# Kernel optimization log

Measured on AMD Instinct MI355X. Metric: run time of the kernel, lower is better.

## Reference

```python
import jax, jax.numpy as jnp
import numpy as np

H = 128  # hidden_dim


def gcn_conv(x, src, dst, n, W, b):
    """PyG GCNConv: add self-loops, symmetric norm, gather-transform-scatter."""
    h = x @ W  # [n, H]
    loop = jnp.arange(n, dtype=src.dtype)
    s = jnp.concatenate([src, loop])
    d = jnp.concatenate([dst, loop])
    deg = jax.ops.segment_sum(jnp.ones(s.shape[0], h.dtype), d, num_segments=n)
    dinv = jnp.where(deg > 0, jax.lax.rsqrt(deg), 0.0)
    norm = dinv[s] * dinv[d]  # [E+n]
    msg = h[s] * norm[:, None]
    out = jax.ops.segment_sum(msg, d, num_segments=n)
    return out + b


def encode(x, edge_index, batch, num_graphs, params):
    src, dst = edge_index[0], edge_index[1]
    n = x.shape[0]
    for (W, b) in params:
        x = jax.nn.relu(gcn_conv(x, src, dst, n, W, b))
    sums = jax.ops.segment_sum(x, batch, num_segments=num_graphs)
    cnts = jax.ops.segment_sum(jnp.ones((n, 1), x.dtype), batch, num_segments=num_graphs)
    return sums / jnp.maximum(cnts, 1.0)  # global_mean_pool -> [B, H]


def setup_inputs() -> dict:
    key = jax.random.key(0)
    ks = jax.random.split(key, 32)
    B, C = 32, 5
    Nd, Ed = 1280, 5120
    Np, Ep = 12800, 204800
    f32 = jnp.float32

    def lin(k, fan_in, fan_out):
        k1, k2 = jax.random.split(k)
        lim = 1.0 / np.sqrt(fan_in)
        W = jax.random.uniform(k1, (fan_in, fan_out), f32, -lim, lim)
        b = jax.random.uniform(k2, (fan_out,), f32, -lim, lim)
        return W, b

    Wd0, bd0 = lin(ks[0], 78, H)
    Wd1, bd1 = lin(ks[1], H, H)
    Wd2, bd2 = lin(ks[2], H, H)
    Wp0, bp0 = lin(ks[3], 1280, H)
    Wp1, bp1 = lin(ks[4], H, H)
    Wp2, bp2 = lin(ks[5], H, H)
    Wq, bq = lin(ks[6], H, H)
    Wk, bk = lin(ks[7], H, H)
    Wv, bv = lin(ks[8], H, H)
    W1, b1 = lin(ks[9], 2 * H, H)
    W2, b2 = lin(ks[10], H, 1)

    drug_x = jax.random.normal(ks[11], (Nd, 78), f32)
    prot_x = jax.random.normal(ks[12], (C, Np, 1280), f32)
    drug_edge_index = jax.random.randint(ks[13], (2, Ed), 0, Nd, jnp.int32)
    prot_edge_index = jax.random.randint(ks[14], (C, 2, Ep), 0, Np, jnp.int32)
    # equal-sized graphs per batch element -> every segment non-empty
    drug_batch = (jnp.arange(Nd, dtype=jnp.int32) * B) // Nd
    prot_batch = (jnp.arange(Np, dtype=jnp.int32) * B) // Np

    return dict(drug_x=drug_x, prot_x=prot_x,
                Wd0=Wd0, bd0=bd0, Wd1=Wd1, bd1=bd1, Wd2=Wd2, bd2=bd2,
                Wp0=Wp0, bp0=bp0, Wp1=Wp1, bp1=bp1, Wp2=Wp2, bp2=bp2,
                Wq=Wq, bq=bq, Wk=Wk, bk=bk, Wv=Wv, bv=bv,
                W1=W1, b1=b1, W2=W2, b2=b2,
                drug_edge_index=drug_edge_index, prot_edge_index=prot_edge_index,
                drug_batch=drug_batch, prot_batch=prot_batch, num_graphs=B)


def reference(drug_x, prot_x, Wd0, bd0, Wd1, bd1, Wd2, bd2,
              Wp0, bp0, Wp1, bp1, Wp2, bp2,
              Wq, bq, Wk, bk, Wv, bv, W1, b1, W2, b2,
              drug_edge_index, prot_edge_index, drug_batch, prot_batch, num_graphs):
    drug_params = [(Wd0, bd0), (Wd1, bd1), (Wd2, bd2)]
    prot_params = [(Wp0, bp0), (Wp1, bp1), (Wp2, bp2)]

    drug_emb = encode(drug_x, drug_edge_index, drug_batch, num_graphs, drug_params)  # [B,H]

    # vmap over conformations -> [C, B, H]
    conf = jax.vmap(lambda x, ei: encode(x, ei, prot_batch, num_graphs, prot_params))(
        prot_x, prot_edge_index)
    conf = jnp.transpose(conf, (1, 0, 2))  # [B, C, H]

    # drug-conditioned cross-attention over conformations
    q = drug_emb @ Wq + bq                      # [B,H]
    keys = conf @ Wk + bk                       # [B,C,H]
    vals = conf @ Wv + bv                       # [B,C,H]
    scores = jnp.einsum('bh,bch->bc', q, keys) / jnp.sqrt(jnp.asarray(H, q.dtype))
    attn = jax.nn.softmax(scores, axis=1)       # [B,C]
    protein_emb = jnp.einsum('bc,bch->bh', attn, vals)

    combined = jnp.concatenate([drug_emb, protein_emb], axis=1)  # [B,2H]
    hidden = jax.nn.relu(combined @ W1 + b1)    # dropout is identity in eval mode
    logits = (hidden @ W2 + b2)[:, 0]           # [B]
    return logits, attn
```

## Files before the change

### kernel.cpp

```cpp
#include <hip/hip_runtime.h>

#define H     128
#define BGR   32
#define NCONF 5
#define ND    1280
#define FD    78
#define ED    5120
#define NP    12800
#define FP    1280
#define EP    204800
#define MAXD  64

#define PROT_GEMM_BLKS 500
#define DRUG_GEMM1_BLKS 20
#define DRUG_GEMM_BLKS 10
#define PLACE_BLKS 4020
#define PROT_MP_BLKS 16000
#define DRUG_MP_BLKS 320

typedef unsigned short u16;
typedef unsigned int   u32;
typedef __attribute__((ext_vector_type(8))) short bf16x8;
typedef __attribute__((ext_vector_type(4))) unsigned int u32x4;
typedef __attribute__((ext_vector_type(4))) unsigned short u16x4;
typedef __attribute__((ext_vector_type(8))) unsigned short u16x8;
typedef __attribute__((ext_vector_type(4))) float f32x4;

__device__ __forceinline__ u16 f2bf(float x) {
  u32 u = __float_as_uint(x);
  u32 r = (u + 0x7FFFu + ((u >> 16) & 1u)) >> 16;
  return (u16)r;
}
__device__ __forceinline__ float bf2f(u16 h) {
  return __uint_as_float(((u32)h) << 16);
}

__device__ __forceinline__ void gload16(const void* gsrc, void* lds) {
  __builtin_amdgcn_global_load_lds(
      (const __attribute__((address_space(1))) unsigned int*)gsrc,
      (__attribute__((address_space(3))) unsigned int*)lds, 16, 0, 0);
}

__device__ __forceinline__ void cvt8(float4 p, float4 q, bf16x8& hi, bf16x8& lo) {
  float f[8] = {p.x, p.y, p.z, p.w, q.x, q.y, q.z, q.w};
  u32x4 h, l;
  #pragma unroll
  for (int j = 0; j < 4; ++j) {
    u32 u0 = __float_as_uint(f[2 * j]);
    u32 u1 = __float_as_uint(f[2 * j + 1]);
    u32 h0 = u0 & 0xFFFF0000u;
    u32 h1 = u1 & 0xFFFF0000u;
    h[j] = (h0 >> 16) | h1;
    float l0 = f[2 * j]     - __uint_as_float(h0);
    float l1 = f[2 * j + 1] - __uint_as_float(h1);
    l[j] = (__float_as_uint(l0) >> 16) | (__float_as_uint(l1) & 0xFFFF0000u);
  }
  union { u32x4 u; bf16x8 b; } ch, cl;
  ch.u = h; cl.u = l;
  hi = ch.b; lo = cl.b;
}

__device__ __forceinline__ void splitW_chunk(
    const float* __restrict__ W, u16* __restrict__ wsW, int K, int g)
{
  int step = g >> 10;
  int r = g & 1023;
  int col = r >> 3, q = r & 7;
  int u = q ^ (col & 7);
  int kc = (u & 3) * 8;
  bool lo = u >= 4;
  int k0 = step * 32 + kc;
  u16x8 o;
  #pragma unroll
  for (int j = 0; j < 8; ++j) {
    float x = W[(size_t)(k0 + j) * 128 + col];
    u16 h = f2bf(x);
    o[j] = lo ? f2bf(x - bf2f(h)) : h;
  }
  *(u16x8*)(wsW + (size_t)g * 8) = o;
}

__global__ __launch_bounds__(256) void splitW_all_k(
    const float* __restrict__ Wp0, const float* __restrict__ Wp1,
    const float* __restrict__ Wp2, const float* __restrict__ Wd1,
    const float* __restrict__ Wd2,
    u16* __restrict__ o0, u16* __restrict__ o1, u16* __restrict__ o2,
    u16* __restrict__ o3, u16* __restrict__ o4,
    int* __restrict__ deg_p, int* __restrict__ deg_d)
{
  int g = blockIdx.x * 256 + threadIdx.x;
  for (int i = g; i < NCONF * NP + ND; i += 224 * 256) {
    if (i < NCONF * NP) deg_p[i] = 0;
    else                deg_d[i - NCONF * NP] = 0;
  }
  if      (g < 40960) splitW_chunk(Wp0, o0, FP, g);
  else if (g < 45056) splitW_chunk(Wp1, o1, H, g - 40960);
  else if (g < 49152) splitW_chunk(Wp2, o2, H, g - 45056);
  else if (g < 53248) splitW_chunk(Wd1, o3, H, g - 49152);
  else if (g < 57344) splitW_chunk(Wd2, o4, H, g - 53248);
}

__device__ __forceinline__ void gemm_pipe_body(
    char* smemRaw, const float* __restrict__ A, const u16* __restrict__ wsW,
    u16* __restrict__ Cout, int K, int blk)
{
  u16* Wlds = (u16*)smemRaw;
  const int t = threadIdx.x;
  const int wid = t >> 6, lane = t & 63;
  const int lane15 = lane & 15, lq = lane >> 4;
  const int m0 = blk * 128;
  const int NT = K >> 5;

  const float* Ar0 = A + (size_t)(m0 + wid * 32 + lane15) * K + lq * 8;
  const float* Ar1 = Ar0 + (size_t)16 * K;
  const u16* sbase = wsW + (size_t)(wid * 4) * 512 + (size_t)lane * 8;

  f32x4 acc[2][8];
  #pragma unroll
  for (int i = 0; i < 2; ++i)
    #pragma unroll
    for (int j = 0; j < 8; ++j)
      acc[i][j] = (f32x4){0.f, 0.f, 0.f, 0.f};

  #define STAGE_W(step, buf) do {                                   \
    const u16* s_ = sbase + (size_t)(step) * 8192;                  \
    u16* d_ = &Wlds[(buf) * 8192 + wid * 2048];                     \
    gload16(s_,        d_);                                         \
    gload16(s_ + 512,  d_ + 512);                                   \
    gload16(s_ + 1024, d_ + 1024);                                  \
    gload16(s_ + 1536, d_ + 1536);                                  \
  } while (0)

  STAGE_W(0, 0);
  asm volatile("" ::: "memory");
  float4 xa0 = *(const float4*)(Ar0);
  float4 xa1 = *(const float4*)(Ar0 + 4);
  float4 xb0 = *(const float4*)(Ar1);
  float4 xb1 = *(const float4*)(Ar1 + 4);
  asm volatile("" ::: "memory");
  float4 ya0 = *(const float4*)(Ar0 + 32);
  float4 ya1 = *(const float4*)(Ar0 + 36);
  float4 yb0 = *(const float4*)(Ar1 + 32);
  float4 yb1 = *(const float4*)(Ar1 + 36);

  #define BODY(T, RA0, RA1, RB0, RB1) do {                                    \
    if ((T) < NT - 1) asm volatile("s_waitcnt vmcnt(4)\ns_barrier" ::: "memory"); \
    else              asm volatile("s_waitcnt vmcnt(0)\ns_barrier"  ::: "memory"); \
    if ((T) + 1 < NT) { STAGE_W((T) + 1, ((T) + 1) & 1); }                    \
    asm volatile("" ::: "memory");                                            \
    bf16x8 ah0, al0, ah1, al1;                                                \
    cvt8(RA0, RA1, ah0, al0);                                                 \
    cvt8(RB0, RB1, ah1, al1);                                                 \
    if ((T) + 2 < NT) {                                                       \
      const float* p0_ = Ar0 + (size_t)((T) + 2) * 32;                        \
      const float* p1_ = Ar1 + (size_t)((T) + 2) * 32;                        \
      RA0 = *(const float4*)(p0_); RA1 = *(const float4*)(p0_ + 4);           \
      RB0 = *(const float4*)(p1_); RB1 = *(const float4*)(p1_ + 4);           \
    }                                                                         \
    const char* base_ = (const char*)&Wlds[((T) & 1) * 8192];                 \
    _Pragma("unroll")                                                         \
    for (int cb = 0; cb < 8; ++cb) {                                          \
      int col_ = cb * 16 + lane15;                                            \
      const char* cbp_ = base_ + col_ * 128;                                  \
      int sw_ = (col_ & 7) << 4;                                              \
      bf16x8 bh_ = *(const bf16x8*)(cbp_ + ((lq << 4) ^ sw_));                \
      bf16x8 bl_ = *(const bf16x8*)(cbp_ + (((lq | 4) << 4) ^ sw_));          \
      acc[0][cb] = __builtin_amdgcn_mfma_f32_16x16x32_bf16(ah0, bh_, acc[0][cb], 0, 0, 0); \
      acc[0][cb] = __builtin_amdgcn_mfma_f32_16x16x32_bf16(al0, bh_, acc[0][cb], 0, 0, 0); \
      acc[0][cb] = __builtin_amdgcn_mfma_f32_16x16x32_bf16(ah0, bl_, acc[0][cb], 0, 0, 0); \
      acc[1][cb] = __builtin_amdgcn_mfma_f32_16x16x32_bf16(ah1, bh_, acc[1][cb], 0, 0, 0); \
      acc[1][cb] = __builtin_amdgcn_mfma_f32_16x16x32_bf16(al1, bh_, acc[1][cb], 0, 0, 0); \
      acc[1][cb] = __builtin_amdgcn_mfma_f32_16x16x32_bf16(ah1, bl_, acc[1][cb], 0, 0, 0); \
    }                                                                         \
  } while (0)

  for (int tt = 0; tt < NT; tt += 2) {
    BODY(tt,     xa0, xa1, xb0, xb1);
    BODY(tt + 1, ya0, ya1, yb0, yb1);
  }
  #undef BODY
  #undef STAGE_W

  #pragma unroll
  for (int rb = 0; rb < 2; ++rb) {
    #pragma unroll
    for (int j = 0; j < 4; ++j) {
      int row = m0 + wid * 32 + rb * 16 + lq * 4 + j;
      u16* Crow = Cout + (size_t)row * 128 + lane15;
      #pragma unroll
      for (int cb = 0; cb < 8; ++cb)
        Crow[cb * 16] = f2bf(acc[rb][cb][j]);
    }
  }
}

__device__ __forceinline__ void gemm_pipe_bf16A_body(
    char* smemRaw, const u16* __restrict__ A, const u16* __restrict__ wsW,
    u16* __restrict__ Cout, int K, int blk)
{
  u16* Wlds = (u16*)smemRaw;
  const int t = threadIdx.x;
  const int wid = t >> 6, lane = t & 63;
  const int lane15 = lane & 15, lq = lane >> 4;
  const int m0 = blk * 128;
  const int NT = K >> 5;

  const u16* Ar0 = A + (size_t)(m0 + wid * 32 + lane15) * K + lq * 8;
  const u16* Ar1 = Ar0 + (size_t)16 * K;
  const u16* sbase = wsW + (size_t)(wid * 4) * 512 + (size_t)lane * 8;

  f32x4 acc[2][8];
  #pragma unroll
  for (int i = 0; i < 2; ++i)
    #pragma unroll
    for (int j = 0; j < 8; ++j)
      acc[i][j] = (f32x4){0.f, 0.f, 0.f, 0.f};

  #define STAGE_W(step, buf) do {                                   \
    const u16* s_ = sbase + (size_t)(step) * 8192;                  \
    u16* d_ = &Wlds[(buf) * 8192 + wid * 2048];                     \
    gload16(s_,        d_);                                         \
    gload16(s_ + 512,  d_ + 512);                                   \
    gload16(s_ + 1024, d_ + 1024);                                  \
    gload16(s_ + 1536, d_ + 1536);                                  \
  } while (0)

  STAGE_W(0, 0);
  asm volatile("" ::: "memory");
  u16x8 xa = *(const u16x8*)(Ar0);
  u16x8 xb = *(const u16x8*)(Ar1);
  asm volatile("" ::: "memory");
  u16x8 ya = *(const u16x8*)(Ar0 + 32);
  u16x8 yb = *(const u16x8*)(Ar1 + 32);

  #define BODYB(T, RA, RB) do {                                               \
    if ((T) < NT - 1) asm volatile("s_waitcnt vmcnt(2)\ns_barrier" ::: "memory"); \
    else              asm volatile("s_waitcnt vmcnt(0)\ns_barrier"  ::: "memory"); \
    if ((T) + 1 < NT) { STAGE_W((T) + 1, ((T) + 1) & 1); }                    \
    asm volatile("" ::: "memory");                                            \
    union { u16x8 u; bf16x8 b; } ca_, cb2_;                                   \
    ca_.u = RA; cb2_.u = RB;                                                  \
    bf16x8 a0 = ca_.b, a1 = cb2_.b;                                           \
    if ((T) + 2 < NT) {                                                       \
      RA = *(const u16x8*)(Ar0 + (size_t)((T) + 2) * 32);                     \
      RB = *(const u16x8*)(Ar1 + (size_t)((T) + 2) * 32);                     \
    }                                                                         \
    const char* base_ = (const char*)&Wlds[((T) & 1) * 8192];                 \
    _Pragma("unroll")                                                         \
    for (int cb = 0; cb < 8; ++cb) {                                          \
      int col_ = cb * 16 + lane15;                                            \
      const char* cbp_ = base_ + col_ * 128;                                  \
      int sw_ = (col_ & 7) << 4;                                              \
      bf16x8 bh_ = *(const bf16x8*)(cbp_ + ((lq << 4) ^ sw_));                \
      bf16x8 bl_ = *(const bf16x8*)(cbp_ + (((lq | 4) << 4) ^ sw_));          \
      acc[0][cb] = __builtin_amdgcn_mfma_f32_16x16x32_bf16(a0, bh_, acc[0][cb], 0, 0, 0); \
      acc[0][cb] = __builtin_amdgcn_mfma_f32_16x16x32_bf16(a0, bl_, acc[0][cb], 0, 0, 0); \
      acc[1][cb] = __builtin_amdgcn_mfma_f32_16x16x32_bf16(a1, bh_, acc[1][cb], 0, 0, 0); \
      acc[1][cb] = __builtin_amdgcn_mfma_f32_16x16x32_bf16(a1, bl_, acc[1][cb], 0, 0, 0); \
    }                                                                         \
  } while (0)

  for (int tt = 0; tt < NT; tt += 2) {
    BODYB(tt,     xa, xb);
    BODYB(tt + 1, ya, yb);
  }
  #undef BODYB
  #undef STAGE_W

  #pragma unroll
  for (int rb = 0; rb < 2; ++rb) {
    #pragma unroll
    for (int j = 0; j < 4; ++j) {
      int row = m0 + wid * 32 + rb * 16 + lq * 4 + j;
      u16* Crow = Cout + (size_t)row * 128 + lane15;
      #pragma unroll
      for (int cb = 0; cb < 8; ++cb)
        Crow[cb * 16] = f2bf(acc[rb][cb][j]);
    }
  }
}

__device__ __forceinline__ void gemm_f32_body(
    char* smemRaw, const float* __restrict__ A, const float* __restrict__ W,
    u16* __restrict__ Cout, int K, int blk)
{
  float* As = (float*)smemRaw;
  float* Bs = (float*)(smemRaw + 16 * 64 * 4);
  const int t = threadIdx.x;
  const int m0 = blk * 64;
  const int colg = (t & 31) * 4;
  const int rowg = (t >> 5) * 8;
  const int rA = t >> 2;
  const int cA = (t & 3) * 4;
  const int rB = t >> 4;
  const int cB = (t & 15) * 4;

  float acc[8][4] = {};

  for (int k0 = 0; k0 < K; k0 += 16) {
    __syncthreads();
    #pragma unroll
    for (int j = 0; j < 4; ++j) {
      int kk = k0 + cA + j;
      As[(cA + j) * 64 + rA] = (kk < K) ? A[(size_t)(m0 + rA) * K + kk] : 0.0f;
    }
    {
      int kk = k0 + rB;
      if (kk < K) {
        *(float4*)&Bs[rB * 128 + cB]      = *(const float4*)(W + (size_t)kk * 128 + cB);
        *(float4*)&Bs[rB * 128 + cB + 64] = *(const float4*)(W + (size_t)kk * 128 + cB + 64);
      } else {
        *(float4*)&Bs[rB * 128 + cB]      = make_float4(0.f, 0.f, 0.f, 0.f);
        *(float4*)&Bs[rB * 128 + cB + 64] = make_float4(0.f, 0.f, 0.f, 0.f);
      }
    }
    __syncthreads();
    #pragma unroll
    for (int k = 0; k < 16; ++k) {
      float4 b  = *(const float4*)&Bs[k * 128 + colg];
      float4 a0 = *(const float4*)&As[k * 64 + rowg];
      float4 a1 = *(const float4*)&As[k * 64 + rowg + 4];
      const float av[8] = {a0.x, a0.y, a0.z, a0.w, a1.x, a1.y, a1.z, a1.w};
      #pragma unroll
      for (int i = 0; i < 8; ++i) {
        acc[i][0] += av[i] * b.x;
        acc[i][1] += av[i] * b.y;
        acc[i][2] += av[i] * b.z;
        acc[i][3] += av[i] * b.w;
      }
    }
  }
  #pragma unroll
  for (int i = 0; i < 8; ++i) {
    u16x4 o;
    o[0] = f2bf(acc[i][0]); o[1] = f2bf(acc[i][1]);
    o[2] = f2bf(acc[i][2]); o[3] = f2bf(acc[i][3]);
    *(u16x4*)(Cout + (size_t)(m0 + rowg + i) * 128 + colg) = o;
  }
}

__global__ __launch_bounds__(256, 4) void stage1_place_k(
    const float* __restrict__ pA, const u16* __restrict__ pW, u16* __restrict__ pC,
    const float* __restrict__ dA, const float* __restrict__ dW, u16* __restrict__ dC,
    const int* __restrict__ prot_ei, const int* __restrict__ drug_ei,
    int* __restrict__ deg_p, u16* __restrict__ slot_p,
    int* __restrict__ deg_d, u16* __restrict__ slot_d)
{
  __shared__ __align__(16) char smem[2 * 16384];
  int b = blockIdx.x;
  if (b < PROT_GEMM_BLKS) {
    gemm_pipe_body(smem, pA, pW, pC, FP, b);
    return;
  }
  b -= PROT_GEMM_BLKS;
  if (b < DRUG_GEMM1_BLKS) {
    gemm_f32_body(smem, dA, dW, dC, FD, b);
    return;
  }
  b -= DRUG_GEMM1_BLKS;
  int idx = b * 256 + threadIdx.x;
  if (idx < NCONF * EP) {
    int c = idx / EP, e = idx - c * EP;
    const int* eic = prot_ei + (size_t)c * 2 * EP;
    int s = eic[e], d = eic[EP + e];
    int node = c * NP + d;
    int pos = atomicAdd(&deg_p[node], 1);
    if (pos < MAXD) slot_p[(size_t)node * MAXD + pos] = (u16)s;
  } else {
    idx -= NCONF * EP;
    if (idx < ED) {
      int s = drug_ei[idx], d = drug_ei[ED + idx];
      int pos = atomicAdd(&deg_d[d], 1);
      if (pos < MAXD) slot_d[(size_t)d * MAXD + pos] = (u16)s;
    }
  }
}

__global__ __launch_bounds__(256, 4) void stage23_gemm_k(
    const u16* __restrict__ pA, const u16* __restrict__ pW, u16* __restrict__ pC,
    const u16* __restrict__ dA, const u16* __restrict__ dW, u16* __restrict__ dC)
{
  __shared__ __align__(16) char smem[2 * 16384];
  if (blockIdx.x < PROT_GEMM_BLKS)
    gemm_pipe_bf16A_body(smem, pA, pW, pC, H, blockIdx.x);
  else
    gemm_pipe_bf16A_body(smem, dA, dW, dC, H, blockIdx.x - PROT_GEMM_BLKS);
}

__device__ __forceinline__ void mp_body(
    const u16* __restrict__ h, u16* __restrict__ xout,
    const int* __restrict__ deg, const u16* __restrict__ slots,
    const float* __restrict__ bias, int wid, int nPer)
{
  int lane = threadIdx.x & 63;
  int c = wid / nPer;
  const int* dg = deg + (size_t)c * nPer;
  int v = wid - c * nPer;
  const u32* hc = (const u32*)(h + (size_t)c * nPer * H);
  const u16* sl = slots + (size_t)wid * MAXD;
  int degv = dg[v];
  float dv = rsqrtf((float)degv + 1.0f);
  u32 us = ((const u32*)h)[(size_t)wid * 64 + lane];
  float a0x = __uint_as_float(us << 16) * dv;
  float a0y = __uint_as_float(us & 0xFFFF0000u) * dv;
  float a1x = 0.f, a1y = 0.f;
  int n = degv < MAXD ? degv : MAXD;
  int i = 0;
  for (; i + 4 <= n; i += 4) {
    int s0 = sl[i], s1 = sl[i + 1], s2 = sl[i + 2], s3 = sl[i + 3];
    float d0 = rsqrtf((float)dg[s0] + 1.0f);
    float d1 = rsqrtf((float)dg[s1] + 1.0f);
    float d2 = rsqrtf((float)dg[s2] + 1.0f);
    float d3 = rsqrtf((float)dg[s3] + 1.0f);
    u32 u0 = hc[(size_t)s0 * 64 + lane];
    u32 u1 = hc[(size_t)s1 * 64 + lane];
    u32 u2 = hc[(size_t)s2 * 64 + lane];
    u32 u3 = hc[(size_t)s3 * 64 + lane];
    a0x += __uint_as_float(u0 << 16) * d0;
    a0y += __uint_as_float(u0 & 0xFFFF0000u) * d0;
    a1x += __uint_as_float(u1 << 16) * d1;
    a1y += __uint_as_float(u1 & 0xFFFF0000u) * d1;
    a0x += __uint_as_float(u2 << 16) * d2;
    a0y += __uint_as_float(u2 & 0xFFFF0000u) * d2;
    a1x += __uint_as_float(u3 << 16) * d3;
    a1y += __uint_as_float(u3 & 0xFFFF0000u) * d3;
  }
  for (; i < n; ++i) {
    int s0 = sl[i];
    float d0 = rsqrtf((float)dg[s0] + 1.0f);
    u32 u0 = hc[(size_t)s0 * 64 + lane];
    a0x += __uint_as_float(u0 << 16) * d0;
    a0y += __uint_as_float(u0 & 0xFFFF0000u) * d0;
  }
  int col = lane * 2;
  float ox = fmaxf((a0x + a1x) * dv + bias[col],     0.0f);
  float oy = fmaxf((a0y + a1y) * dv + bias[col + 1], 0.0f);
  u32 ow = (u32)f2bf(ox) | ((u32)f2bf(oy) << 16);
  ((u32*)xout)[(size_t)wid * 64 + lane] = ow;
}

__global__ __launch_bounds__(256) void mp_all_k(
    const u16* __restrict__ hp, u16* __restrict__ xp,
    const int* __restrict__ degp, const u16* __restrict__ slotp,
    const float* __restrict__ biasp,
    const u16* __restrict__ hd, u16* __restrict__ xd,
    const int* __restrict__ degd, const u16* __restrict__ slotd,
    const float* __restrict__ biasd)
{
  int blk = blockIdx.x;
  int wv = threadIdx.x >> 6;
  if (blk < PROT_MP_BLKS) {
    mp_body(hp, xp, degp, slotp, biasp, blk * 4 + wv, NP);
  } else {
    mp_body(hd, xd, degd, slotd, biasd, (blk - PROT_MP_BLKS) * 4 + wv, ND);
  }
}

__device__ __forceinline__ void pool_body(
    const u16* __restrict__ x, float* __restrict__ out, int blk, int npg)
{
  __shared__ float part[4][128];
  const int col = threadIdx.x & 127;
  const int rp  = threadIdx.x >> 7;
  size_t row0 = (size_t)blk * npg;
  float acc = 0.0f;
  for (int i = rp; i < npg; i += 4)
    acc += bf2f(x[(row0 + i) * H + col]);
  part[rp][col] = acc;
  __syncthreads();
  if (rp == 0)
    out[(size_t)blk * H + col] =
        (part[0][col] + part[1][col] + part[2][col] + part[3][col]) / (float)npg;
}

__global__ __launch_bounds__(512) void pool_all_k(
    const u16* __restrict__ xd, float* __restrict__ outd,
    const u16* __restrict__ xp, float* __restrict__ outp)
{
  if (blockIdx.x < BGR) pool_body(xd, outd, blockIdx.x, ND / BGR);
  else                  pool_body(xp, outp, blockIdx.x - BGR, NP / BGR);
}

__global__ __launch_bounds__(128) void attn_mlp_k(
    const float* __restrict__ drug_emb, const float* __restrict__ conf_pool,
    const float* __restrict__ Wq, const float* __restrict__ bq,
    const float* __restrict__ Wk, const float* __restrict__ bk,
    const float* __restrict__ Wv, const float* __restrict__ bv,
    const float* __restrict__ W1, const float* __restrict__ b1,
    const float* __restrict__ W2, const float* __restrict__ b2,
    float* __restrict__ out)
{
  const int b = blockIdx.x;
  const int hcol = threadIdx.x;
  __shared__ float de[H], pc[H], vals_s[NCONF][H], red[H], sc[NCONF], peS[H];

  de[hcol] = drug_emb[(size_t)b * H + hcol];
  __syncthreads();

  float qv = bq[hcol];
  for (int k = 0; k < H; ++k) qv += de[k] * Wq[k * H + hcol];

  for (int c = 0; c < NCONF; ++c) {
    __syncthreads();
    pc[hcol] = conf_pool[((size_t)c * BGR + b) * H + hcol];
    __syncthreads();
    float kk = bk[hcol], vv = bv[hcol];
    for (int k = 0; k < H; ++k) {
      float p = pc[k];
      kk += p * Wk[k * H + hcol];
      vv += p * Wv[k * H + hcol];
    }
    vals_s[c][hcol] = vv;
    red[hcol] = qv * kk;
    __syncthreads();
    for (int s = 64; s > 0; s >>= 1) {
      if (hcol < s) red[hcol] += red[hcol + s];
      __syncthreads();
    }
    if (hcol == 0) sc[c] = red[0] * 0.08838834764831845f;
  }
  __syncthreads();

  float m = sc[0];
  for (int c = 1; c < NCONF; ++c) m = fmaxf(m, sc[c]);
  float ex[NCONF], sum = 0.0f;
  for (int c = 0; c < NCONF; ++c) { ex[c] = expf(sc[c] - m); sum += ex[c]; }
  float inv = 1.0f / sum;
  if (hcol < NCONF) out[BGR + b * NCONF + hcol] = ex[hcol] * inv;

  float pe = 0.0f;
  for (int c = 0; c < NCONF; ++c) pe += (ex[c] * inv) * vals_s[c][hcol];
  peS[hcol] = pe;
  __syncthreads();

  float hid = b1[hcol];
  for (int k = 0; k < H; ++k) hid += de[k]  * W1[k * H + hcol];
  for (int k = 0; k < H; ++k) hid += peS[k] * W1[(H + k) * H + hcol];
  hid = fmaxf(hid, 0.0f);

  red[hcol] = hid * W2[hcol];
  __syncthreads();
  for (int s = 64; s > 0; s >>= 1) {
    if (hcol < s) red[hcol] += red[hcol + s];
    __syncthreads();
  }
  if (hcol == 0) out[b] = red[0] + b2[0];
}

extern "C" void kernel_launch(void* const* d_in, const int* in_sizes, int n_in,
                              void* d_out, int out_size, void* d_ws, size_t ws_size,
                              hipStream_t stream)
{
  const float* drug_x  = (const float*)d_in[0];
  const float* prot_x  = (const float*)d_in[1];
  const float* Wd0 = (const float*)d_in[2];  const float* bd0 = (const float*)d_in[3];
  const float* Wd1 = (const float*)d_in[4];  const float* bd1 = (const float*)d_in[5];
  const float* Wd2 = (const float*)d_in[6];  const float* bd2 = (const float*)d_in[7];
  const float* Wp0 = (const float*)d_in[8];  const float* bp0 = (const float*)d_in[9];
  const float* Wp1 = (const float*)d_in[10]; const float* bp1 = (const float*)d_in[11];
  const float* Wp2 = (const float*)d_in[12]; const float* bp2 = (const float*)d_in[13];
  const float* Wq  = (const float*)d_in[14]; const float* bq  = (const float*)d_in[15];
  const float* Wk  = (const float*)d_in[16]; const float* bk  = (const float*)d_in[17];
  const float* Wv  = (const float*)d_in[18]; const float* bv  = (const float*)d_in[19];
  const float* W1  = (const float*)d_in[20]; const float* b1  = (const float*)d_in[21];
  const float* W2  = (const float*)d_in[22]; const float* b2  = (const float*)d_in[23];
  const int* drug_ei = (const int*)d_in[24];
  const int* prot_ei = (const int*)d_in[25];
  float* out = (float*)d_out;

  char* base = (char*)d_ws;
  size_t off = 0;
  auto alloc = [&](size_t bytes) -> char* {
    char* p = base + off;
    off = (off + bytes + 255) & ~(size_t)255;
    return p;
  };
  int*   deg_p   = (int*)  alloc((size_t)NCONF * NP * 4);
  int*   deg_d   = (int*)  alloc((size_t)ND * 4);
  u16*   slot_p  = (u16*)  alloc((size_t)NCONF * NP * MAXD * 2);
  u16*   slot_d  = (u16*)  alloc((size_t)ND * MAXD * 2);
  u16*   bufHp   = (u16*)  alloc((size_t)NCONF * NP * H * 2);
  u16*   bufXp   = (u16*)  alloc((size_t)NCONF * NP * H * 2);
  u16*   bufHd   = (u16*)  alloc((size_t)ND * H * 2);
  u16*   bufXd   = (u16*)  alloc((size_t)ND * H * 2);
  float* drugemb = (float*)alloc((size_t)BGR * H * 4);
  float* confp   = (float*)alloc((size_t)NCONF * BGR * H * 4);
  u16* Wp0ws = (u16*)alloc((size_t)FP * 512);
  u16* Wp1ws = (u16*)alloc((size_t)H * 512);
  u16* Wp2ws = (u16*)alloc((size_t)H * 512);
  u16* Wd1ws = (u16*)alloc((size_t)H * 512);
  u16* Wd2ws = (u16*)alloc((size_t)H * 512);

  splitW_all_k<<<224, 256, 0, stream>>>(Wp0, Wp1, Wp2, Wd1, Wd2,
                                        Wp0ws, Wp1ws, Wp2ws, Wd1ws, Wd2ws,
                                        deg_p, deg_d);

  stage1_place_k<<<PROT_GEMM_BLKS + DRUG_GEMM1_BLKS + PLACE_BLKS, 256, 0, stream>>>(
      prot_x, Wp0ws, bufHp, drug_x, Wd0, bufHd,
      prot_ei, drug_ei, deg_p, slot_p, deg_d, slot_d);

  mp_all_k<<<PROT_MP_BLKS + DRUG_MP_BLKS, 256, 0, stream>>>(
      bufHp, bufXp, deg_p, slot_p, bp0,
      bufHd, bufXd, deg_d, slot_d, bd0);
  stage23_gemm_k<<<PROT_GEMM_BLKS + DRUG_GEMM_BLKS, 256, 0, stream>>>(
      bufXp, Wp1ws, bufHp, bufXd, Wd1ws, bufHd);
  mp_all_k<<<PROT_MP_BLKS + DRUG_MP_BLKS, 256, 0, stream>>>(
      bufHp, bufXp, deg_p, slot_p, bp1,
      bufHd, bufXd, deg_d, slot_d, bd1);
  stage23_gemm_k<<<PROT_GEMM_BLKS + DRUG_GEMM_BLKS, 256, 0, stream>>>(
      bufXp, Wp2ws, bufHp, bufXd, Wd2ws, bufHd);
  mp_all_k<<<PROT_MP_BLKS + DRUG_MP_BLKS, 256, 0, stream>>>(
      bufHp, bufXp, deg_p, slot_p, bp2,
      bufHd, bufXd, deg_d, slot_d, bd2);

  pool_all_k<<<BGR + NCONF * BGR, 512, 0, stream>>>(bufXd, drugemb, bufXp, confp);

  attn_mlp_k<<<BGR, 128, 0, stream>>>(drugemb, confp, Wq, bq, Wk, bk, Wv, bv,
                                      W1, b1, W2, b2, out);
}
```

Before: 391.4 us.

## Use 64-row tiles for protein layer-1 GEMM and swizzle MP block order

The first protein GEMM (K=1280) now uses 64-row M tiles instead of 128, so it launches 1000 blocks rather than 500, each wave holding one 16-row strip. The intent is more parallelism and lower register use to fill the CUs better, at the cost of reloading the weight tiles from global memory twice as often. Separately, the message-passing kernel remaps block IDs in an XCD-style stride-8 pattern so that consecutive nodes land on the same chiplet, aiming for better L2 locality. The remap assumes the grid size divides by 8, which holds here (16320).

```diff
diff --git a/kernel.cpp b/kernel.cpp
--- a/kernel.cpp
+++ b/kernel.cpp
@@ -11,6 +11,7 @@
 #define EP    204800
 #define MAXD  64
 
+#define PROT_GEMM1_BLKS 1000
 #define PROT_GEMM_BLKS 500
 #define DRUG_GEMM1_BLKS 20
 #define DRUG_GEMM_BLKS 10
@@ -100,7 +101,7 @@
   else if (g < 57344) splitW_chunk(Wd2, o4, H, g - 53248);
 }
 
-__device__ __forceinline__ void gemm_pipe_body(
+__device__ __forceinline__ void gemm_pipe64_body(
     char* smemRaw, const float* __restrict__ A, const u16* __restrict__ wsW,
     u16* __restrict__ Cout, int K, int blk)
 {
@@ -108,19 +109,15 @@
   const int t = threadIdx.x;
   const int wid = t >> 6, lane = t & 63;
   const int lane15 = lane & 15, lq = lane >> 4;
-  const int m0 = blk * 128;
+  const int m0 = blk * 64;
   const int NT = K >> 5;
 
-  const float* Ar0 = A + (size_t)(m0 + wid * 32 + lane15) * K + lq * 8;
-  const float* Ar1 = Ar0 + (size_t)16 * K;
+  const float* Ar = A + (size_t)(m0 + wid * 16 + lane15) * K + lq * 8;
   const u16* sbase = wsW + (size_t)(wid * 4) * 512 + (size_t)lane * 8;
 
-  f32x4 acc[2][8];
+  f32x4 acc[8];
   #pragma unroll
-  for (int i = 0; i < 2; ++i)
-    #pragma unroll
-    for (int j = 0; j < 8; ++j)
-      acc[i][j] = (f32x4){0.f, 0.f, 0.f, 0.f};
+  for (int j = 0; j < 8; ++j) acc[j] = (f32x4){0.f, 0.f, 0.f, 0.f};
 
   #define STAGE_W(step, buf) do {                                   \
     const u16* s_ = sbase + (size_t)(step) * 8192;                  \
@@ -133,29 +130,22 @@
 
   STAGE_W(0, 0);
   asm volatile("" ::: "memory");
-  float4 xa0 = *(const float4*)(Ar0);
-  float4 xa1 = *(const float4*)(Ar0 + 4);
-  float4 xb0 = *(const float4*)(Ar1);
-  float4 xb1 = *(const float4*)(Ar1 + 4);
+  float4 xa0 = *(const float4*)(Ar);
+  float4 xa1 = *(const float4*)(Ar + 4);
   asm volatile("" ::: "memory");
-  float4 ya0 = *(const float4*)(Ar0 + 32);
-  float4 ya1 = *(const float4*)(Ar0 + 36);
-  float4 yb0 = *(const float4*)(Ar1 + 32);
-  float4 yb1 = *(const float4*)(Ar1 + 36);
-
-  #define BODY(T, RA0, RA1, RB0, RB1) do {                                    \
-    if ((T) < NT - 1) asm volatile("s_waitcnt vmcnt(4)\ns_barrier" ::: "memory"); \
+  float4 ya0 = *(const float4*)(Ar + 32);
+  float4 ya1 = *(const float4*)(Ar + 36);
+
+  #define BODY64(T, RA0, RA1) do {                                            \
+    if ((T) < NT - 1) asm volatile("s_waitcnt vmcnt(2)\ns_barrier" ::: "memory"); \
     else              asm volatile("s_waitcnt vmcnt(0)\ns_barrier"  ::: "memory"); \
     if ((T) + 1 < NT) { STAGE_W((T) + 1, ((T) + 1) & 1); }                    \
     asm volatile("" ::: "memory");                                            \
-    bf16x8 ah0, al0, ah1, al1;                                                \
-    cvt8(RA0, RA1, ah0, al0);                                                 \
-    cvt8(RB0, RB1, ah1, al1);                                                 \
+    bf16x8 ah, al;                                                            \
+    cvt8(RA0, RA1, ah, al);                                                   \
     if ((T) + 2 < NT) {                                                       \
-      const float* p0_ = Ar0 + (size_t)((T) + 2) * 32;                        \
-      const float* p1_ = Ar1 + (size_t)((T) + 2) * 32;                        \
-      RA0 = *(const float4*)(p0_); RA1 = *(const float4*)(p0_ + 4);           \
-      RB0 = *(const float4*)(p1_); RB1 = *(const float4*)(p1_ + 4);           \
+      const float* p_ = Ar + (size_t)((T) + 2) * 32;                          \
+      RA0 = *(const float4*)(p_); RA1 = *(const float4*)(p_ + 4);             \
     }                                                                         \
     const char* base_ = (const char*)&Wlds[((T) & 1) * 8192];                 \
     _Pragma("unroll")                                                         \
@@ -165,32 +155,26 @@
       int sw_ = (col_ & 7) << 4;                                              \
       bf16x8 bh_ = *(const bf16x8*)(cbp_ + ((lq << 4) ^ sw_));                \
       bf16x8 bl_ = *(const bf16x8*)(cbp_ + (((lq | 4) << 4) ^ sw_));          \
-      acc[0][cb] = __builtin_amdgcn_mfma_f32_16x16x32_bf16(ah0, bh_, acc[0][cb], 0, 0, 0); \
-      acc[0][cb] = __builtin_amdgcn_mfma_f32_16x16x32_bf16(al0, bh_, acc[0][cb], 0, 0, 0); \
-      acc[0][cb] = __builtin_amdgcn_mfma_f32_16x16x32_bf16(ah0, bl_, acc[0][cb], 0, 0, 0); \
-      acc[1][cb] = __builtin_amdgcn_mfma_f32_16x16x32_bf16(ah1, bh_, acc[1][cb], 0, 0, 0); \
-      acc[1][cb] = __builtin_amdgcn_mfma_f32_16x16x32_bf16(al1, bh_, acc[1][cb], 0, 0, 0); \
-      acc[1][cb] = __builtin_amdgcn_mfma_f32_16x16x32_bf16(ah1, bl_, acc[1][cb], 0, 0, 0); \
+      acc[cb] = __builtin_amdgcn_mfma_f32_16x16x32_bf16(ah, bh_, acc[cb], 0, 0, 0); \
+      acc[cb] = __builtin_amdgcn_mfma_f32_16x16x32_bf16(al, bh_, acc[cb], 0, 0, 0); \
+      acc[cb] = __builtin_amdgcn_mfma_f32_16x16x32_bf16(ah, bl_, acc[cb], 0, 0, 0); \
     }                                                                         \
   } while (0)
 
   for (int tt = 0; tt < NT; tt += 2) {
-    BODY(tt,     xa0, xa1, xb0, xb1);
-    BODY(tt + 1, ya0, ya1, yb0, yb1);
-  }
-  #undef BODY
+    BODY64(tt,     xa0, xa1);
+    BODY64(tt + 1, ya0, ya1);
+  }
+  #undef BODY64
   #undef STAGE_W
 
   #pragma unroll
-  for (int rb = 0; rb < 2; ++rb) {
+  for (int j = 0; j < 4; ++j) {
+    int row = m0 + wid * 16 + lq * 4 + j;
+    u16* Crow = Cout + (size_t)row * 128 + lane15;
     #pragma unroll
-    for (int j = 0; j < 4; ++j) {
-      int row = m0 + wid * 32 + rb * 16 + lq * 4 + j;
-      u16* Crow = Cout + (size_t)row * 128 + lane15;
-      #pragma unroll
-      for (int cb = 0; cb < 8; ++cb)
-        Crow[cb * 16] = f2bf(acc[rb][cb][j]);
-    }
+    for (int cb = 0; cb < 8; ++cb)
+      Crow[cb * 16] = f2bf(acc[cb][j]);
   }
 }
 
@@ -348,11 +332,11 @@
 {
   __shared__ __align__(16) char smem[2 * 16384];
   int b = blockIdx.x;
-  if (b < PROT_GEMM_BLKS) {
-    gemm_pipe_body(smem, pA, pW, pC, FP, b);
+  if (b < PROT_GEMM1_BLKS) {
+    gemm_pipe64_body(smem, pA, pW, pC, FP, b);
     return;
   }
-  b -= PROT_GEMM_BLKS;
+  b -= PROT_GEMM1_BLKS;
   if (b < DRUG_GEMM1_BLKS) {
     gemm_f32_body(smem, dA, dW, dC, FD, b);
     return;
@@ -447,12 +431,14 @@
     const int* __restrict__ degd, const u16* __restrict__ slotd,
     const float* __restrict__ biasd)
 {
-  int blk = blockIdx.x;
+  int bid = blockIdx.x;
+  int cpx = gridDim.x >> 3;
+  bid = (bid & 7) * cpx + (bid >> 3);
   int wv = threadIdx.x >> 6;
-  if (blk < PROT_MP_BLKS) {
-    mp_body(hp, xp, degp, slotp, biasp, blk * 4 + wv, NP);
+  if (bid < PROT_MP_BLKS) {
+    mp_body(hp, xp, degp, slotp, biasp, bid * 4 + wv, NP);
   } else {
-    mp_body(hd, xd, degd, slotd, biasd, (blk - PROT_MP_BLKS) * 4 + wv, ND);
+    mp_body(hd, xd, degd, slotd, biasd, (bid - PROT_MP_BLKS) * 4 + wv, ND);
   }
 }
 
@@ -595,7 +581,7 @@
                                         Wp0ws, Wp1ws, Wp2ws, Wd1ws, Wd2ws,
                                         deg_p, deg_d);
 
-  stage1_place_k<<<PROT_GEMM_BLKS + DRUG_GEMM1_BLKS + PLACE_BLKS, 256, 0, stream>>>(
+  stage1_place_k<<<PROT_GEMM1_BLKS + DRUG_GEMM1_BLKS + PLACE_BLKS, 256, 0, stream>>>(
       prot_x, Wp0ws, bufHp, drug_x, Wd0, bufHd,
       prot_ei, drug_ei, deg_p, slot_p, deg_d, slot_d);
 
```

After: 371.5 us. 5.1% less time.
